# Kernel tuning notes

Measured on AMD Instinct MI355X. Metric: run time of the kernel, lower is better.

Reference implementation:

```python
import jax, jax.numpy as jnp
import numpy as np

B, S, HID = 1, 2048, 2880
H, KV, D = 64, 8, 64
WINDOW = 128
SCALE = D ** -0.5
NEG_INF = jnp.float32(-1e30)


def _rope_cos_sin():
    # realistic RoPE tables over full head_dim (HF rotate_half convention)
    inv_freq = 1.0 / (10000.0 ** (np.arange(0, D, 2, dtype=np.float32) / D))
    t = np.arange(S, dtype=np.float32)
    freqs = np.outer(t, inv_freq)                      # [S, D/2]
    emb = np.concatenate([freqs, freqs], axis=-1)      # [S, D]
    return jnp.asarray(np.cos(emb))[None], jnp.asarray(np.sin(emb))[None]


def setup_inputs() -> dict:
    key = jax.random.key(0)
    ks = jax.random.split(key, 10)
    cos, sin = _rope_cos_sin()
    sd = lambda fan_in: 1.0 / np.sqrt(fan_in)
    return {
        "hidden_states": jax.random.normal(ks[0], (B, S, HID), jnp.float32),
        "cos": cos, "sin": sin,
        "Wq": jax.random.normal(ks[1], (HID, H * D), jnp.float32) * sd(HID),
        "bq": jax.random.normal(ks[2], (H * D,), jnp.float32) * 0.02,
        "Wk": jax.random.normal(ks[3], (HID, KV * D), jnp.float32) * sd(HID),
        "bk": jax.random.normal(ks[4], (KV * D,), jnp.float32) * 0.02,
        "Wv": jax.random.normal(ks[5], (HID, KV * D), jnp.float32) * sd(HID),
        "bv": jax.random.normal(ks[6], (KV * D,), jnp.float32) * 0.02,
        "Wo": jax.random.normal(ks[7], (H * D, HID), jnp.float32) * sd(H * D),
        "bo": jax.random.normal(ks[8], (HID,), jnp.float32) * 0.02,
        "sinks": jax.random.normal(ks[9], (H,), jnp.float32),
    }


def _rotate_half(x):
    x1, x2 = jnp.split(x, 2, axis=-1)
    return jnp.concatenate([-x2, x1], axis=-1)


def _forward(hidden_states, cos, sin, Wq, bq, Wk, bk, Wv, bv, Wo, bo, sinks):
    q = (hidden_states @ Wq + bq).reshape(B, S, H, D)
    k = (hidden_states @ Wk + bk).reshape(B, S, KV, D)
    v = (hidden_states @ Wv + bv).reshape(B, S, KV, D)
    # RoPE with explicit cos/sin, unsqueeze at head dim (bsnd layout)
    c, s = cos[:, :, None, :], sin[:, :, None, :]
    q = q * c + _rotate_half(q) * s
    k = k * c + _rotate_half(k) * s
    # GQA: expand kv heads to match query heads
    k = jnp.repeat(k, H // KV, axis=2)
    v = jnp.repeat(v, H // KV, axis=2)
    scores = jnp.einsum("bqhd,bkhd->bhqk", q, k) * SCALE  # [B,H,S,S]
    i = jnp.arange(S)[:, None]
    j = jnp.arange(S)[None, :]
    allowed = (j <= i) & (j > i - WINDOW)                  # causal + sliding window
    scores = jnp.where(allowed, scores, NEG_INF)
    # sink-augmented softmax: sinks act as an extra logit per head, dropped after norm
    m = jnp.maximum(scores.max(axis=-1), sinks[None, :, None])  # [B,H,S]
    p = jnp.exp(scores - m[..., None])                      # [B,H,S,S]
    denom = p.sum(axis=-1) + jnp.exp(sinks[None, :, None] - m)  # [B,H,S]
    attn = jnp.einsum("bhqk,bkhd->bqhd", p, v) / denom.transpose(0, 2, 1)[..., None]
    return attn.reshape(B, S, H * D) @ Wo + bo


def reference(hidden_states, cos, sin, Wq, bq, Wk, bk, Wv, bv, Wo, bo, sinks):
    return _forward(hidden_states, cos, sin, Wq, bq, Wk, bk, Wv, bv, Wo, bo, sinks)
```

## Files before the change

kernel.cpp:

```cpp
#include <hip/hip_runtime.h>

typedef unsigned short u16;
typedef __bf16 bf16x8 __attribute__((ext_vector_type(8)));
typedef float f32x4 __attribute__((ext_vector_type(4)));

constexpr int SEQ = 2048;
constexpr int HIDN = 2880;
constexpr int NQKV = 5120;
constexpr float SCALE = 0.125f;
constexpr float NEG_INF = -1e30f;

__device__ __forceinline__ u16 f2bf(float f) {
  unsigned int u = __builtin_bit_cast(unsigned int, f);
  u += 0x7FFFu + ((u >> 16) & 1u);
  return (u16)(u >> 16);
}
__device__ __forceinline__ float bf2f(u16 h) {
  unsigned int u = ((unsigned int)h) << 16;
  return __builtin_bit_cast(float, u);
}
__device__ __forceinline__ void async_load16(const void* g, void* l) {
  __builtin_amdgcn_global_load_lds(
      (const __attribute__((address_space(1))) unsigned int*)g,
      (__attribute__((address_space(3))) unsigned int*)l, 16, 0, 0);
}

__global__ __launch_bounds__(256) void conv_f2b(const float* __restrict__ in,
                                                u16* __restrict__ out, long n4) {
  long i = (long)blockIdx.x * 256 + threadIdx.x;
  if (i >= n4) return;
  float4 v = ((const float4*)in)[i];
  u16 o0 = f2bf(v.x), o1 = f2bf(v.y), o2 = f2bf(v.z), o3 = f2bf(v.w);
  out[i * 4 + 0] = o0; out[i * 4 + 1] = o1; out[i * 4 + 2] = o2; out[i * 4 + 3] = o3;
}

__global__ __launch_bounds__(256) void transpose_qkv(const float* __restrict__ Wq,
                                                     const float* __restrict__ Wk,
                                                     const float* __restrict__ Wv,
                                                     u16* __restrict__ out) {
  __shared__ float tile[32][33];
  int c0 = blockIdx.x * 32, r0 = blockIdx.y * 32;
  int tx = threadIdx.x & 31, ty = threadIdx.x >> 5;
  const float* src; int C, cl;
  if (c0 < 4096)      { src = Wq; C = 4096; cl = c0; }
  else if (c0 < 4608) { src = Wk; C = 512;  cl = c0 - 4096; }
  else                { src = Wv; C = 512;  cl = c0 - 4608; }
#pragma unroll
  for (int i = 0; i < 32; i += 8)
    tile[ty + i][tx] = src[(long)(r0 + ty + i) * C + cl + tx];
  __syncthreads();
#pragma unroll
  for (int i = 0; i < 32; i += 8)
    out[(long)(c0 + ty + i) * HIDN + r0 + tx] = f2bf(tile[tx][ty + i]);
}

__global__ __launch_bounds__(256) void transpose_f2b(const float* __restrict__ in,
                                                     u16* __restrict__ out,
                                                     int R, int C, int ostride) {
  __shared__ float tile[32][33];
  int c0 = blockIdx.x * 32, r0 = blockIdx.y * 32;
  int tx = threadIdx.x & 31, ty = threadIdx.x >> 5;
#pragma unroll
  for (int i = 0; i < 32; i += 8)
    tile[ty + i][tx] = in[(long)(r0 + ty + i) * C + c0 + tx];
  __syncthreads();
#pragma unroll
  for (int i = 0; i < 32; i += 8)
    out[(long)(c0 + ty + i) * ostride + r0 + tx] = f2bf(tile[tx][ty + i]);
}

__global__ __launch_bounds__(256) void concat_bias(const float* bq, const float* bk,
                                                   const float* bv, float* out) {
  int t = blockIdx.x * 256 + threadIdx.x;
  if (t < 4096) out[t] = bq[t];
  else if (t < 4608) out[t] = bk[t - 4096];
  else if (t < 5120) out[t] = bv[t - 4608];
}

template <int MODE>
__global__ __launch_bounds__(256, 2) void gemm_db(const u16* __restrict__ A,
                                                  const u16* __restrict__ Bp,
                                                  const float* __restrict__ bias,
                                                  const float* __restrict__ cosb,
                                                  const float* __restrict__ sinb,
                                                  void* __restrict__ out0,
                                                  int N, int Kst, int nkt) {
  __shared__ u16 lds[32768];
  const int tid = threadIdx.x, lane = tid & 63, wid = tid >> 6;
  const int wm = wid >> 1, wn = wid & 1;
  const int lr = lane & 15, lk = lane >> 4;

  const int gm = gridDim.x;
  int nwg = gm * gridDim.y;
  int bid = blockIdx.y * gm + blockIdx.x;
  int q8 = nwg >> 3, r8 = nwg & 7;
  int xcd = bid & 7, seq = bid >> 3;
  int swz = (xcd < r8 ? xcd * (q8 + 1) : r8 * (q8 + 1) + (xcd - r8) * q8) + seq;
  const long brow = (long)(swz % gm) * 128;
  const long bcol = (long)(swz / gm) * 128;

  char* L = (char*)lds;
  const int kc8 = ((tid & 3) ^ ((tid >> 3) & 3)) * 8;
  const u16* As[2];
  const u16* Bs[2];
#pragma unroll
  for (int i = 0; i < 2; ++i) {
    int c = tid + 256 * i;
    As[i] = A  + (brow + (c >> 2)) * (long)Kst + kc8;
    Bs[i] = Bp + (bcol + (c >> 2)) * (long)Kst + kc8;
  }
  auto stage = [&](int kt, int b) {
    char* d = L + b * 32768;
    long ko = (long)kt * 64;
#pragma unroll
    for (int i = 0; i < 2; ++i) {
      async_load16(As[i] + ko,      d +         i * 4096 + tid * 16);
      async_load16(As[i] + ko + 32, d +  8192 + i * 4096 + tid * 16);
      async_load16(Bs[i] + ko,      d + 16384 + i * 4096 + tid * 16);
      async_load16(Bs[i] + ko + 32, d + 24576 + i * 4096 + tid * 16);
    }
  };

  const int phys = (lk ^ ((lr >> 1) & 3)) << 4;
  const int arow = (wm * 64 + lr) * 64 + phys;
  const int brow_ = (wn * 64 + lr) * 64 + phys;

  f32x4 acc[4][4] = {};
  stage(0, 0);
  __syncthreads();

  for (int t = 0; t < nkt; ++t) {
    const char* Lb = L + (t & 1) * 32768;
    bf16x8 a0[4], b0[4], a1[4], b1[4];
#pragma unroll
    for (int m = 0; m < 4; ++m) a0[m] = *(const bf16x8*)(Lb + arow + m * 1024);
#pragma unroll
    for (int n = 0; n < 4; ++n) b0[n] = *(const bf16x8*)(Lb + 16384 + brow_ + n * 1024);
#pragma unroll
    for (int m = 0; m < 4; ++m) a1[m] = *(const bf16x8*)(Lb + 8192 + arow + m * 1024);
#pragma unroll
    for (int n = 0; n < 4; ++n) b1[n] = *(const bf16x8*)(Lb + 24576 + brow_ + n * 1024);
    if (t + 1 < nkt) stage(t + 1, (t & 1) ^ 1);
#pragma unroll
    for (int m = 0; m < 4; ++m)
#pragma unroll
      for (int n = 0; n < 4; ++n)
        acc[m][n] = __builtin_amdgcn_mfma_f32_16x16x32_bf16(a0[m], b0[n], acc[m][n], 0, 0, 0);
#pragma unroll
    for (int m = 0; m < 4; ++m)
#pragma unroll
      for (int n = 0; n < 4; ++n)
        acc[m][n] = __builtin_amdgcn_mfma_f32_16x16x32_bf16(a1[m], b1[n], acc[m][n], 0, 0, 0);
    __syncthreads();
  }

  const int col0 = (int)bcol + wn * 64;
  if (MODE == 0) {
    const bool rope = (col0 < 4608);
#pragma unroll
    for (int mf = 0; mf < 4; ++mf) {
      long row = brow + wm * 64 + mf * 16 + lk * 4;
#pragma unroll
      for (int r = 0; r < 4; ++r) {
        long s = row + r;
        if (rope) {
#pragma unroll
          for (int nf = 0; nf < 2; ++nf) {
            int col = col0 + nf * 16 + lr;
            int d = nf * 16 + lr;
            float c = cosb[s * 64 + d], sn = sinb[s * 64 + d];
            float x1 = acc[mf][nf][r] + bias[col];
            float x2 = acc[mf][nf + 2][r] + bias[col + 32];
            ((u16*)out0)[s * (long)N + col]      = f2bf(x1 * c - x2 * sn);
            ((u16*)out0)[s * (long)N + col + 32] = f2bf(x2 * c + x1 * sn);
          }
        } else {
#pragma unroll
          for (int nf = 0; nf < 4; ++nf) {
            int col = col0 + nf * 16 + lr;
            ((u16*)out0)[s * (long)N + col] = f2bf(acc[mf][nf][r] + bias[col]);
          }
        }
      }
    }
  } else {
#pragma unroll
    for (int mf = 0; mf < 4; ++mf) {
      long row = brow + wm * 64 + mf * 16 + lk * 4;
#pragma unroll
      for (int nf = 0; nf < 4; ++nf) {
        int col = col0 + nf * 16 + lr;
        if (col < N) {
          float bv = bias[col];
#pragma unroll
          for (int r = 0; r < 4; ++r)
            ((float*)out0)[(row + r) * (long)N + col] = acc[mf][nf][r] + bv;
        }
      }
    }
  }
}

__global__ __launch_bounds__(256, 1) void attn_kernel(const u16* __restrict__ QKV,
                                                      const float* __restrict__ sinks,
                                                      u16* __restrict__ Oa) {
  __shared__ u16 Ks[64 * 64];
  __shared__ u16 Vt[64 * 64];
  __shared__ u16 Ps[4][64 * 72];
  const int tid = threadIdx.x, wid = tid >> 6, lane = tid & 63;
  const int lr = lane & 15, lk = lane >> 4;
  const int i0 = blockIdx.x * 64;
  const int h = blockIdx.y * 4 + wid;
  const int g = h >> 3;

  bf16x8 qf[4][2];
#pragma unroll
  for (int m = 0; m < 4; ++m)
#pragma unroll
    for (int kc = 0; kc < 2; ++kc)
      qf[m][kc] = *(const bf16x8*)&QKV[(long)(i0 + m * 16 + lr) * NQKV + h * 64 + kc * 32 + lk * 8];

  const float sinkh = sinks[h];
  float mrun[4][4], lrun[4][4];
  f32x4 oacc[4][4] = {};
#pragma unroll
  for (int m = 0; m < 4; ++m)
#pragma unroll
    for (int r = 0; r < 4; ++r) { mrun[m][r] = sinkh; lrun[m][r] = 0.f; }

  const int jb0 = (i0 >= 128) ? (i0 - 128) : 0;
  for (int jb = jb0; jb <= i0; jb += 64) {
#pragma unroll
    for (int i = 0; i < 2; ++i) {
      int c = wid * 128 + i * 64 + lane;
      int row = c >> 3, sp = c & 7;
      int ssrc = sp ^ (row & 7);
      async_load16(QKV + (long)(jb + row) * NQKV + 4096 + g * 64 + ssrc * 8,
                   ((char*)Ks) + c * 16);
    }
    {
      int j0 = (tid & 31) * 2, d0 = (tid >> 5) * 8;
      const u16* vp = QKV + (long)(jb + j0) * NQKV + 4608 + g * 64 + d0;
      int4 rv0 = *(const int4*)vp;
      int4 rv1 = *(const int4*)(vp + NQKV);
      const u16* a0 = (const u16*)&rv0;
      const u16* a1 = (const u16*)&rv1;
#pragma unroll
      for (int e = 0; e < 8; ++e) {
        int d = d0 + e;
        unsigned val = (unsigned)a0[e] | ((unsigned)a1[e] << 16);
        int byt = d * 128 + ((((j0 >> 3) ^ (d & 7)) << 4)) + ((j0 & 7) * 2);
        *(unsigned*)((char*)Vt + byt) = val;
      }
    }
    __syncthreads();

    f32x4 sf[4][4] = {};
    __builtin_amdgcn_s_setprio(1);
#pragma unroll
    for (int kc = 0; kc < 2; ++kc) {
      bf16x8 kf[4];
#pragma unroll
      for (int cf = 0; cf < 4; ++cf) {
        int row = cf * 16 + lr;
        kf[cf] = *(const bf16x8*)((const char*)Ks + row * 128 + (((kc * 4 + lk) ^ (lr & 7)) << 4));
      }
#pragma unroll
      for (int m = 0; m < 4; ++m)
#pragma unroll
        for (int cf = 0; cf < 4; ++cf)
          sf[m][cf] = __builtin_amdgcn_mfma_f32_16x16x32_bf16(qf[m][kc], kf[cf], sf[m][cf], 0, 0, 0);
    }
    __builtin_amdgcn_s_setprio(0);

#pragma unroll
    for (int m = 0; m < 4; ++m) {
      float rmax[4];
#pragma unroll
      for (int r = 0; r < 4; ++r) {
        int i = i0 + m * 16 + lk * 4 + r;
        float mx = NEG_INF;
#pragma unroll
        for (int cf = 0; cf < 4; ++cf) {
          int j = jb + cf * 16 + lr;
          float v = sf[m][cf][r] * SCALE;
          bool ok = (j <= i) && (j > i - 128);
          v = ok ? v : NEG_INF;
          sf[m][cf][r] = v;
          mx = fmaxf(mx, v);
        }
#pragma unroll
        for (int off = 1; off < 16; off <<= 1) mx = fmaxf(mx, __shfl_xor(mx, off, 64));
        rmax[r] = mx;
      }
#pragma unroll
      for (int r = 0; r < 4; ++r) {
        float mnew = fmaxf(mrun[m][r], rmax[r]);
        float corr = __expf(mrun[m][r] - mnew);
        mrun[m][r] = mnew;
        float rsum = 0.f;
#pragma unroll
        for (int cf = 0; cf < 4; ++cf) {
          float p = __expf(sf[m][cf][r] - mnew);
          sf[m][cf][r] = p;
          rsum += p;
        }
#pragma unroll
        for (int off = 1; off < 16; off <<= 1) rsum += __shfl_xor(rsum, off, 64);
        lrun[m][r] = lrun[m][r] * corr + rsum;
#pragma unroll
        for (int dn = 0; dn < 4; ++dn) oacc[m][dn][r] *= corr;
      }
    }

#pragma unroll
    for (int m = 0; m < 4; ++m)
#pragma unroll
      for (int cf = 0; cf < 4; ++cf)
#pragma unroll
        for (int r = 0; r < 4; ++r)
          Ps[wid][(m * 16 + lk * 4 + r) * 72 + cf * 16 + lr] = f2bf(sf[m][cf][r]);
    __syncthreads();

    __builtin_amdgcn_s_setprio(1);
#pragma unroll
    for (int kc = 0; kc < 2; ++kc) {
      bf16x8 pf[4], vf[4];
#pragma unroll
      for (int m = 0; m < 4; ++m)
        pf[m] = *(const bf16x8*)&Ps[wid][(m * 16 + lr) * 72 + kc * 32 + lk * 8];
#pragma unroll
      for (int dn = 0; dn < 4; ++dn) {
        int row = dn * 16 + lr;
        vf[dn] = *(const bf16x8*)((const char*)Vt + row * 128 + (((kc * 4 + lk) ^ (lr & 7)) << 4));
      }
#pragma unroll
      for (int m = 0; m < 4; ++m)
#pragma unroll
        for (int dn = 0; dn < 4; ++dn)
          oacc[m][dn] = __builtin_amdgcn_mfma_f32_16x16x32_bf16(pf[m], vf[dn], oacc[m][dn], 0, 0, 0);
    }
    __builtin_amdgcn_s_setprio(0);
    __syncthreads();
  }

#pragma unroll
  for (int m = 0; m < 4; ++m)
#pragma unroll
    for (int r = 0; r < 4; ++r) {
      float denom = lrun[m][r] + __expf(sinkh - mrun[m][r]);
      float inv = 1.f / denom;
      long row = i0 + m * 16 + lk * 4 + r;
#pragma unroll
      for (int dn = 0; dn < 4; ++dn)
        Oa[row * 4096 + h * 64 + dn * 16 + lr] = f2bf(oacc[m][dn][r] * inv);
    }
}

extern "C" void kernel_launch(void* const* d_in, const int* in_sizes, int n_in,
                              void* d_out, int out_size, void* d_ws, size_t ws_size,
                              hipStream_t stream) {
  const float* X    = (const float*)d_in[0];
  const float* cosb = (const float*)d_in[1];
  const float* sinb = (const float*)d_in[2];
  const float* Wq   = (const float*)d_in[3];
  const float* bq   = (const float*)d_in[4];
  const float* Wk   = (const float*)d_in[5];
  const float* bk   = (const float*)d_in[6];
  const float* Wv   = (const float*)d_in[7];
  const float* bv   = (const float*)d_in[8];
  const float* Wo   = (const float*)d_in[9];
  const float* bo   = (const float*)d_in[10];
  const float* sinks = (const float*)d_in[11];

  char* ws = (char*)d_ws;
  size_t off = 0;
  auto alloc = [&](size_t bytes) -> void* {
    void* p = ws + off;
    off += (bytes + 255) & ~(size_t)255;
    return p;
  };
  u16*   Xb    = (u16*)alloc((size_t)SEQ * HIDN * 2);
  u16*   Wqkv  = (u16*)alloc((size_t)NQKV * HIDN * 2);
  u16*   Wot   = (u16*)alloc((size_t)2944 * 4096 * 2);
  float* bqkv  = (float*)alloc((size_t)NQKV * 4);
  u16*   QKV   = (u16*)alloc((size_t)SEQ * NQKV * 2);
  u16*   Ab    = (u16*)alloc((size_t)SEQ * 4096 * 2);
  (void)ws_size; (void)in_sizes; (void)n_in; (void)out_size;

  conv_f2b<<<(SEQ * HIDN / 4 + 255) / 256, 256, 0, stream>>>(X, Xb, (long)SEQ * HIDN / 4);
  transpose_qkv<<<dim3(NQKV / 32, HIDN / 32), 256, 0, stream>>>(Wq, Wk, Wv, Wqkv);
  transpose_f2b<<<dim3(HIDN / 32, 4096 / 32), 256, 0, stream>>>(Wo, Wot, 4096, HIDN, 4096);
  concat_bias<<<(NQKV + 255) / 256, 256, 0, stream>>>(bq, bk, bv, bqkv);
  gemm_db<0><<<dim3(16, 40), 256, 0, stream>>>(Xb, Wqkv, bqkv, cosb, sinb,
                                               QKV, NQKV, HIDN, 45);
  attn_kernel<<<dim3(SEQ / 64, 64 / 4), 256, 0, stream>>>(QKV, sinks, Ab);
  gemm_db<1><<<dim3(16, 23), 256, 0, stream>>>(Ab, Wot, bo, nullptr, nullptr,
                                               d_out, HIDN, 4096, 64);
}
```

Measured before the change: 264.4 us.

## Use 256x128 GEMM tiles with K=32 stages and split-K for output projection

The GEMM tile grows from 128x128 to 256x128 and the K-step per stage drops from 64 to 32, which shrinks double-buffered LDS to 48KB while each wave does 8x4 MFMAs per step. The output projection now uses 2-way split-K over blockIdx.z, writing partials to d_out and to a scratch buffer that reuses the QKV weight workspace. A new combine kernel adds the two partials and the bias. The aim is more data reuse per tile and enough blocks for the output GEMM to fill the CUs, at the cost of an extra full-size fp32 read/write pass and higher register pressure from the 32 accumulators.

```diff
diff --git a/kernel.cpp b/kernel.cpp
--- a/kernel.cpp
+++ b/kernel.cpp
@@ -9,6 +9,7 @@
 constexpr int NQKV = 5120;
 constexpr float SCALE = 0.125f;
 constexpr float NEG_INF = -1e30f;
+constexpr int BUFSTRIDE = 24576;
 
 __device__ __forceinline__ u16 f2bf(float f) {
   unsigned int u = __builtin_bit_cast(unsigned int, f);
@@ -78,14 +79,15 @@
 }
 
 template <int MODE>
-__global__ __launch_bounds__(256, 2) void gemm_db(const u16* __restrict__ A,
-                                                  const u16* __restrict__ Bp,
-                                                  const float* __restrict__ bias,
-                                                  const float* __restrict__ cosb,
-                                                  const float* __restrict__ sinb,
-                                                  void* __restrict__ out0,
-                                                  int N, int Kst, int nkt) {
-  __shared__ u16 lds[32768];
+__global__ __launch_bounds__(256, 2) void gemm_v10(const u16* __restrict__ A,
+                                                   const u16* __restrict__ Bp,
+                                                   const float* __restrict__ bias,
+                                                   const float* __restrict__ cosb,
+                                                   const float* __restrict__ sinb,
+                                                   void* __restrict__ out0,
+                                                   float* __restrict__ out1,
+                                                   int N, int Kst, int nkt) {
+  __shared__ u16 lds[24576];
   const int tid = threadIdx.x, lane = tid & 63, wid = tid >> 6;
   const int wm = wid >> 1, wn = wid & 1;
   const int lr = lane & 15, lk = lane >> 4;
@@ -96,61 +98,52 @@
   int q8 = nwg >> 3, r8 = nwg & 7;
   int xcd = bid & 7, seq = bid >> 3;
   int swz = (xcd < r8 ? xcd * (q8 + 1) : r8 * (q8 + 1) + (xcd - r8) * q8) + seq;
-  const long brow = (long)(swz % gm) * 128;
+  const long brow = (long)(swz % gm) * 256;
   const long bcol = (long)(swz / gm) * 128;
+  const long kbase = (MODE == 1) ? (long)blockIdx.z * nkt * 32 : 0;
 
   char* L = (char*)lds;
   const int kc8 = ((tid & 3) ^ ((tid >> 3) & 3)) * 8;
-  const u16* As[2];
+  const u16* As[4];
   const u16* Bs[2];
 #pragma unroll
-  for (int i = 0; i < 2; ++i) {
-    int c = tid + 256 * i;
-    As[i] = A  + (brow + (c >> 2)) * (long)Kst + kc8;
-    Bs[i] = Bp + (bcol + (c >> 2)) * (long)Kst + kc8;
-  }
+  for (int i = 0; i < 4; ++i)
+    As[i] = A + (brow + ((tid + 256 * i) >> 2)) * (long)Kst + kbase + kc8;
+#pragma unroll
+  for (int i = 0; i < 2; ++i)
+    Bs[i] = Bp + (bcol + ((tid + 256 * i) >> 2)) * (long)Kst + kbase + kc8;
   auto stage = [&](int kt, int b) {
-    char* d = L + b * 32768;
-    long ko = (long)kt * 64;
-#pragma unroll
-    for (int i = 0; i < 2; ++i) {
-      async_load16(As[i] + ko,      d +         i * 4096 + tid * 16);
-      async_load16(As[i] + ko + 32, d +  8192 + i * 4096 + tid * 16);
-      async_load16(Bs[i] + ko,      d + 16384 + i * 4096 + tid * 16);
-      async_load16(Bs[i] + ko + 32, d + 24576 + i * 4096 + tid * 16);
-    }
+    char* d = L + b * BUFSTRIDE;
+    long ko = (long)kt * 32;
+#pragma unroll
+    for (int i = 0; i < 4; ++i)
+      async_load16(As[i] + ko, d + (tid + 256 * i) * 16);
+#pragma unroll
+    for (int i = 0; i < 2; ++i)
+      async_load16(Bs[i] + ko, d + 16384 + (tid + 256 * i) * 16);
   };
 
   const int phys = (lk ^ ((lr >> 1) & 3)) << 4;
-  const int arow = (wm * 64 + lr) * 64 + phys;
-  const int brow_ = (wn * 64 + lr) * 64 + phys;
-
-  f32x4 acc[4][4] = {};
+  const int arow = (wm * 128 + lr) * 64 + phys;
+  const int brw  = 16384 + (wn * 64 + lr) * 64 + phys;
+
+  f32x4 acc[8][4] = {};
   stage(0, 0);
   __syncthreads();
 
   for (int t = 0; t < nkt; ++t) {
-    const char* Lb = L + (t & 1) * 32768;
-    bf16x8 a0[4], b0[4], a1[4], b1[4];
-#pragma unroll
-    for (int m = 0; m < 4; ++m) a0[m] = *(const bf16x8*)(Lb + arow + m * 1024);
-#pragma unroll
-    for (int n = 0; n < 4; ++n) b0[n] = *(const bf16x8*)(Lb + 16384 + brow_ + n * 1024);
-#pragma unroll
-    for (int m = 0; m < 4; ++m) a1[m] = *(const bf16x8*)(Lb + 8192 + arow + m * 1024);
-#pragma unroll
-    for (int n = 0; n < 4; ++n) b1[n] = *(const bf16x8*)(Lb + 24576 + brow_ + n * 1024);
+    const char* Lb = L + (t & 1) * BUFSTRIDE;
+    bf16x8 a[8], b[4];
+#pragma unroll
+    for (int m = 0; m < 8; ++m) a[m] = *(const bf16x8*)(Lb + arow + m * 1024);
+#pragma unroll
+    for (int n = 0; n < 4; ++n) b[n] = *(const bf16x8*)(Lb + brw + n * 1024);
     if (t + 1 < nkt) stage(t + 1, (t & 1) ^ 1);
 #pragma unroll
-    for (int m = 0; m < 4; ++m)
+    for (int m = 0; m < 8; ++m)
 #pragma unroll
       for (int n = 0; n < 4; ++n)
-        acc[m][n] = __builtin_amdgcn_mfma_f32_16x16x32_bf16(a0[m], b0[n], acc[m][n], 0, 0, 0);
-#pragma unroll
-    for (int m = 0; m < 4; ++m)
-#pragma unroll
-      for (int n = 0; n < 4; ++n)
-        acc[m][n] = __builtin_amdgcn_mfma_f32_16x16x32_bf16(a1[m], b1[n], acc[m][n], 0, 0, 0);
+        acc[m][n] = __builtin_amdgcn_mfma_f32_16x16x32_bf16(a[m], b[n], acc[m][n], 0, 0, 0);
     __syncthreads();
   }
 
@@ -158,8 +151,8 @@
   if (MODE == 0) {
     const bool rope = (col0 < 4608);
 #pragma unroll
-    for (int mf = 0; mf < 4; ++mf) {
-      long row = brow + wm * 64 + mf * 16 + lk * 4;
+    for (int mf = 0; mf < 8; ++mf) {
+      long row = brow + wm * 128 + mf * 16 + lk * 4;
 #pragma unroll
       for (int r = 0; r < 4; ++r) {
         long s = row + r;
@@ -184,21 +177,36 @@
       }
     }
   } else {
-#pragma unroll
-    for (int mf = 0; mf < 4; ++mf) {
-      long row = brow + wm * 64 + mf * 16 + lk * 4;
+    float* o = (blockIdx.z == 0) ? (float*)out0 : out1;
+#pragma unroll
+    for (int mf = 0; mf < 8; ++mf) {
+      long row = brow + wm * 128 + mf * 16 + lk * 4;
 #pragma unroll
       for (int nf = 0; nf < 4; ++nf) {
         int col = col0 + nf * 16 + lr;
         if (col < N) {
-          float bv = bias[col];
 #pragma unroll
           for (int r = 0; r < 4; ++r)
-            ((float*)out0)[(row + r) * (long)N + col] = acc[mf][nf][r] + bv;
+            o[(row + r) * (long)N + col] = acc[mf][nf][r];
         }
       }
     }
   }
+}
+
+__global__ __launch_bounds__(256) void combine_out(const float* __restrict__ P1,
+                                                   const float* __restrict__ bias,
+                                                   float* __restrict__ out) {
+  long i = (long)blockIdx.x * 256 + threadIdx.x;
+  if (i >= (long)SEQ * HIDN / 4) return;
+  int c4 = (int)(i % (HIDN / 4));
+  float4 p0 = ((const float4*)out)[i];
+  float4 p1 = ((const float4*)P1)[i];
+  float4 b = ((const float4*)bias)[c4];
+  float4 r;
+  r.x = p0.x + p1.x + b.x; r.y = p0.y + p1.y + b.y;
+  r.z = p0.z + p1.z + b.z; r.w = p0.w + p1.w + b.w;
+  ((float4*)out)[i] = r;
 }
 
 __global__ __launch_bounds__(256, 1) void attn_kernel(const u16* __restrict__ QKV,
@@ -386,15 +394,17 @@
   float* bqkv  = (float*)alloc((size_t)NQKV * 4);
   u16*   QKV   = (u16*)alloc((size_t)SEQ * NQKV * 2);
   u16*   Ab    = (u16*)alloc((size_t)SEQ * 4096 * 2);
+  float* Pt1 = (float*)Wqkv;
   (void)ws_size; (void)in_sizes; (void)n_in; (void)out_size;
 
   conv_f2b<<<(SEQ * HIDN / 4 + 255) / 256, 256, 0, stream>>>(X, Xb, (long)SEQ * HIDN / 4);
   transpose_qkv<<<dim3(NQKV / 32, HIDN / 32), 256, 0, stream>>>(Wq, Wk, Wv, Wqkv);
   transpose_f2b<<<dim3(HIDN / 32, 4096 / 32), 256, 0, stream>>>(Wo, Wot, 4096, HIDN, 4096);
   concat_bias<<<(NQKV + 255) / 256, 256, 0, stream>>>(bq, bk, bv, bqkv);
-  gemm_db<0><<<dim3(16, 40), 256, 0, stream>>>(Xb, Wqkv, bqkv, cosb, sinb,
-                                               QKV, NQKV, HIDN, 45);
+  gemm_v10<0><<<dim3(8, 40, 1), 256, 0, stream>>>(Xb, Wqkv, bqkv, cosb, sinb,
+                                                  QKV, nullptr, NQKV, HIDN, 90);
   attn_kernel<<<dim3(SEQ / 64, 64 / 4), 256, 0, stream>>>(QKV, sinks, Ab);
-  gemm_db<1><<<dim3(16, 23), 256, 0, stream>>>(Ab, Wot, bo, nullptr, nullptr,
-                                               d_out, HIDN, 4096, 64);
-}
+  gemm_v10<1><<<dim3(8, 23, 2), 256, 0, stream>>>(Ab, Wot, nullptr, nullptr, nullptr,
+                                                  d_out, Pt1, HIDN, 4096, 64);
+  combine_out<<<(SEQ * HIDN / 4 + 255) / 256, 256, 0, stream>>>(Pt1, bo, (float*)d_out);
+}
```

New measurement: 253.7 us. 1.04x faster.

## Use per-wave private LDS tiles in GEMMs to eliminate workgroup barriers

Applied to the files above, without the earlier changes.

Restructures both GEMMs so each wave asynchronously loads its own 64-row A and B slices into a private double-buffered LDS region with a K-step of 32. Synchronization uses explicit vmcnt/lgkmcnt waits instead of __syncthreads, and MFMA priority is raised. This is meant to remove block-wide barrier stalls, at the cost of duplicated global/L2 loads across waves and twice as many loop iterations.

```diff
diff --git a/kernel.cpp b/kernel.cpp
--- a/kernel.cpp
+++ b/kernel.cpp
@@ -10,6 +10,10 @@
 constexpr float SCALE = 0.125f;
 constexpr float NEG_INF = -1e30f;
 
+#define ASM_VMCNT(n)  asm volatile("s_waitcnt vmcnt(" #n ")" ::: "memory")
+#define ASM_LGKM(n)   asm volatile("s_waitcnt lgkmcnt(" #n ")" ::: "memory")
+#define SCHEDBAR()    __builtin_amdgcn_sched_barrier(0)
+
 __device__ __forceinline__ u16 f2bf(float f) {
   unsigned int u = __builtin_bit_cast(unsigned int, f);
   u += 0x7FFFu + ((u >> 16) & 1u);
@@ -24,6 +28,12 @@
       (const __attribute__((address_space(1))) unsigned int*)g,
       (__attribute__((address_space(3))) unsigned int*)l, 16, 0, 0);
 }
+__device__ __forceinline__ f32x4 DSR(unsigned addr) {
+  f32x4 d;
+  asm volatile("ds_read_b128 %0, %1" : "=v"(d) : "v"(addr));
+  return d;
+}
+__device__ __forceinline__ bf16x8 asbf(f32x4 v) { return __builtin_bit_cast(bf16x8, v); }
 
 __global__ __launch_bounds__(256) void conv_f2b(const float* __restrict__ in,
                                                 u16* __restrict__ out, long n4) {
@@ -78,7 +88,7 @@
 }
 
 template <int MODE>
-__global__ __launch_bounds__(256, 2) void gemm_db(const u16* __restrict__ A,
+__global__ __launch_bounds__(256, 2) void gemm_nb(const u16* __restrict__ A,
                                                   const u16* __restrict__ Bp,
                                                   const float* __restrict__ bias,
                                                   const float* __restrict__ cosb,
@@ -100,58 +110,54 @@
   const long bcol = (long)(swz / gm) * 128;
 
   char* L = (char*)lds;
-  const int kc8 = ((tid & 3) ^ ((tid >> 3) & 3)) * 8;
-  const u16* As[2];
-  const u16* Bs[2];
-#pragma unroll
-  for (int i = 0; i < 2; ++i) {
-    int c = tid + 256 * i;
-    As[i] = A  + (brow + (c >> 2)) * (long)Kst + kc8;
-    Bs[i] = Bp + (bcol + (c >> 2)) * (long)Kst + kc8;
+  char* Wb = L + wid * 16384;
+
+  const int kc8 = ((lane & 3) ^ ((lane >> 3) & 3)) * 8;
+  const u16* As[4];
+  const u16* Bs[4];
+#pragma unroll
+  for (int i = 0; i < 4; ++i) {
+    int row = i * 16 + (lane >> 2);
+    As[i] = A  + (brow + wm * 64 + row) * (long)Kst + kc8;
+    Bs[i] = Bp + (bcol + wn * 64 + row) * (long)Kst + kc8;
   }
   auto stage = [&](int kt, int b) {
-    char* d = L + b * 32768;
-    long ko = (long)kt * 64;
-#pragma unroll
-    for (int i = 0; i < 2; ++i) {
-      async_load16(As[i] + ko,      d +         i * 4096 + tid * 16);
-      async_load16(As[i] + ko + 32, d +  8192 + i * 4096 + tid * 16);
-      async_load16(Bs[i] + ko,      d + 16384 + i * 4096 + tid * 16);
-      async_load16(Bs[i] + ko + 32, d + 24576 + i * 4096 + tid * 16);
+    char* d = Wb + b * 8192;
+    long ko = (long)kt * 32;
+#pragma unroll
+    for (int i = 0; i < 4; ++i) {
+      async_load16(As[i] + ko, d +        i * 1024 + lane * 16);
+      async_load16(Bs[i] + ko, d + 4096 + i * 1024 + lane * 16);
     }
   };
 
-  const int phys = (lk ^ ((lr >> 1) & 3)) << 4;
-  const int arow = (wm * 64 + lr) * 64 + phys;
-  const int brow_ = (wn * 64 + lr) * 64 + phys;
+  const unsigned lds0 = (unsigned)(size_t)Wb;
+  const unsigned phys = (unsigned)((lk ^ ((lr >> 1) & 3)) << 4);
+  const unsigned aoff = lds0 + (unsigned)(lr * 64) + phys;
+  const unsigned boff = lds0 + 4096u + (unsigned)(lr * 64) + phys;
 
   f32x4 acc[4][4] = {};
   stage(0, 0);
-  __syncthreads();
 
   for (int t = 0; t < nkt; ++t) {
-    const char* Lb = L + (t & 1) * 32768;
-    bf16x8 a0[4], b0[4], a1[4], b1[4];
-#pragma unroll
-    for (int m = 0; m < 4; ++m) a0[m] = *(const bf16x8*)(Lb + arow + m * 1024);
-#pragma unroll
-    for (int n = 0; n < 4; ++n) b0[n] = *(const bf16x8*)(Lb + 16384 + brow_ + n * 1024);
-#pragma unroll
-    for (int m = 0; m < 4; ++m) a1[m] = *(const bf16x8*)(Lb + 8192 + arow + m * 1024);
-#pragma unroll
-    for (int n = 0; n < 4; ++n) b1[n] = *(const bf16x8*)(Lb + 24576 + brow_ + n * 1024);
-    if (t + 1 < nkt) stage(t + 1, (t & 1) ^ 1);
+    const int b = t & 1;
+    if (t + 1 < nkt) { stage(t + 1, b ^ 1); ASM_VMCNT(8); }
+    else             { ASM_VMCNT(0); }
+    const unsigned ab = aoff + (unsigned)(b * 8192);
+    const unsigned bb = boff + (unsigned)(b * 8192);
+    f32x4 a[4], bf4[4];
+#pragma unroll
+    for (int m = 0; m < 4; ++m) a[m] = DSR(ab + m * 1024u);
+#pragma unroll
+    for (int n = 0; n < 4; ++n) bf4[n] = DSR(bb + n * 1024u);
+    ASM_LGKM(0); SCHEDBAR();
+    __builtin_amdgcn_s_setprio(1);
 #pragma unroll
     for (int m = 0; m < 4; ++m)
 #pragma unroll
       for (int n = 0; n < 4; ++n)
-        acc[m][n] = __builtin_amdgcn_mfma_f32_16x16x32_bf16(a0[m], b0[n], acc[m][n], 0, 0, 0);
-#pragma unroll
-    for (int m = 0; m < 4; ++m)
-#pragma unroll
-      for (int n = 0; n < 4; ++n)
-        acc[m][n] = __builtin_amdgcn_mfma_f32_16x16x32_bf16(a1[m], b1[n], acc[m][n], 0, 0, 0);
-    __syncthreads();
+        acc[m][n] = __builtin_amdgcn_mfma_f32_16x16x32_bf16(asbf(a[m]), asbf(bf4[n]), acc[m][n], 0, 0, 0);
+    __builtin_amdgcn_s_setprio(0);
   }
 
   const int col0 = (int)bcol + wn * 64;
@@ -392,9 +398,9 @@
   transpose_qkv<<<dim3(NQKV / 32, HIDN / 32), 256, 0, stream>>>(Wq, Wk, Wv, Wqkv);
   transpose_f2b<<<dim3(HIDN / 32, 4096 / 32), 256, 0, stream>>>(Wo, Wot, 4096, HIDN, 4096);
   concat_bias<<<(NQKV + 255) / 256, 256, 0, stream>>>(bq, bk, bv, bqkv);
-  gemm_db<0><<<dim3(16, 40), 256, 0, stream>>>(Xb, Wqkv, bqkv, cosb, sinb,
-                                               QKV, NQKV, HIDN, 45);
+  gemm_nb<0><<<dim3(16, 40), 256, 0, stream>>>(Xb, Wqkv, bqkv, cosb, sinb,
+                                               QKV, NQKV, HIDN, 90);
   attn_kernel<<<dim3(SEQ / 64, 64 / 4), 256, 0, stream>>>(QKV, sinks, Ab);
-  gemm_db<1><<<dim3(16, 23), 256, 0, stream>>>(Ab, Wot, bo, nullptr, nullptr,
-                                               d_out, HIDN, 4096, 64);
-}
+  gemm_nb<1><<<dim3(16, 23), 256, 0, stream>>>(Ab, Wot, bo, nullptr, nullptr,
+                                               d_out, HIDN, 4096, 128);
+}
```

Result: slower. 341.8 us (+29.3%).
